# Optimization experiments

Measured on AMD Instinct MI355X. Metric: run time of the kernel, lower is better.

Reference implementation:

```python
import jax, jax.numpy as jnp
import numpy as np

N_NODES = 50000


def _mlp(h, W1, b1, W2, b2):
    return jax.nn.relu(h @ W1.T + b1) @ W2.T + b2


def _gine_layer(h, src, dst, e_emb):
    # messages: ReLU(x_src + edge_embedding), summed at destination (PyG GINEConv, eps=0)
    m = jax.nn.relu(h[src] + e_emb)                       # [E, D]
    agg = jax.ops.segment_sum(m, dst, num_segments=N_NODES)
    return h + agg                                         # (1+eps)*x + agg, eps=0


def setup_inputs() -> dict:
    key = jax.random.key(0)
    ks = jax.random.split(key, 20)
    N, E = N_NODES, 800000
    in_dim, hid, edim, n_types = 64, 128, 16, 100
    s = 0.05
    inp = {
        "x": jax.random.normal(ks[0], (N, in_dim), jnp.float32),
        "edge_index": jax.random.randint(ks[1], (2, E), 0, N, jnp.int64),
        "edge_attr": jax.random.normal(ks[2], (E, edim), jnp.float32),
        "edge_weights": jax.random.uniform(ks[3], (E,), jnp.float32),
        # layer 1: edge lin edim->in_dim, node MLP in_dim->hid->hid
        "We1": jax.random.normal(ks[4], (in_dim, edim), jnp.float32) * s,
        "be1": jnp.zeros((in_dim,), jnp.float32),
        "W11": jax.random.normal(ks[5], (hid, in_dim), jnp.float32) * s,
        "b11": jnp.zeros((hid,), jnp.float32),
        "W12": jax.random.normal(ks[6], (hid, hid), jnp.float32) * s,
        "b12": jnp.zeros((hid,), jnp.float32),
        # layer 2: edge lin edim->hid, node MLP hid->hid->hid
        "We2": jax.random.normal(ks[7], (hid, edim), jnp.float32) * s,
        "be2": jnp.zeros((hid,), jnp.float32),
        "W21": jax.random.normal(ks[8], (hid, hid), jnp.float32) * s,
        "b21": jnp.zeros((hid,), jnp.float32),
        "W22": jax.random.normal(ks[9], (hid, hid), jnp.float32) * s,
        "b22": jnp.zeros((hid,), jnp.float32),
        # output head hid -> n_atom_types
        "Wo": jax.random.normal(ks[10], (n_types, hid), jnp.float32) * s,
        "bo": jnp.zeros((n_types,), jnp.float32),
    }
    return inp


def reference(x, edge_index, edge_attr, edge_weights,
              We1, be1, W11, b11, W12, b12,
              We2, be2, W21, b21, W22, b22,
              Wo, bo):
    src, dst = edge_index[0], edge_index[1]
    ea = edge_attr * edge_weights[:, None]                 # per-edge scaling
    # layer 1
    h = _gine_layer(x, src, dst, ea @ We1.T + be1)
    h = jax.nn.relu(_mlp(h, W11, b11, W12, b12))
    # layer 2
    h = _gine_layer(h, src, dst, ea @ We2.T + be2)
    h = jax.nn.relu(_mlp(h, W21, b21, W22, b22))
    return h @ Wo.T + bo
```

## Files before the change

### kernel.cpp

```cpp
#include <hip/hip_runtime.h>

#define N_NODES 50000
#define E_EDGES 800000
#define SCAN_NB 196

__global__ __launch_bounds__(256) void k_hist(
    const int* __restrict__ ei, int* __restrict__ cnt)
{
    const int e = blockIdx.x * 256 + threadIdx.x;
    if (e < E_EDGES) atomicAdd(&cnt[ei[E_EDGES + e]], 1);
}

__global__ __launch_bounds__(256) void k_scan1(
    const int* __restrict__ cnt, int* __restrict__ bsum)
{
    __shared__ int red[256];
    const int tid = threadIdx.x;
    const int i = blockIdx.x * 256 + tid;
    red[tid] = (i < N_NODES) ? cnt[i] : 0;
    __syncthreads();
    for (int off = 128; off > 0; off >>= 1) {
        if (tid < off) red[tid] += red[tid + off];
        __syncthreads();
    }
    if (tid == 0) bsum[blockIdx.x] = red[0];
}

__global__ __launch_bounds__(256) void k_scan2(
    const int* __restrict__ bsum, int* __restrict__ boff)
{
    __shared__ int part[256];
    const int tid = threadIdx.x;
    const int v = (tid < SCAN_NB) ? bsum[tid] : 0;
    part[tid] = v;
    __syncthreads();
    for (int off = 1; off < 256; off <<= 1) {
        const int vv = part[tid];
        const int u = (tid >= off) ? part[tid - off] : 0;
        __syncthreads();
        part[tid] = vv + u;
        __syncthreads();
    }
    if (tid < SCAN_NB) boff[tid] = part[tid] - v;
}

__global__ __launch_bounds__(256) void k_scan3(
    const int* __restrict__ cnt, const int* __restrict__ boff,
    int* __restrict__ rowptr, int* __restrict__ cursor)
{
    __shared__ int part[256];
    const int tid = threadIdx.x;
    const int i = blockIdx.x * 256 + tid;
    const int v = (i < N_NODES) ? cnt[i] : 0;
    part[tid] = v;
    __syncthreads();
    for (int off = 1; off < 256; off <<= 1) {
        const int vv = part[tid];
        const int u = (tid >= off) ? part[tid - off] : 0;
        __syncthreads();
        part[tid] = vv + u;
        __syncthreads();
    }
    const int excl = part[tid] - v + boff[blockIdx.x];
    if (i < N_NODES) { rowptr[i] = excl; cursor[i] = excl; }
    if (i == N_NODES) rowptr[N_NODES] = excl;
}

__global__ __launch_bounds__(256) void k_scatter(
    const int* __restrict__ ei, int* __restrict__ cursor, int2* __restrict__ pairs)
{
    const int e = blockIdx.x * 256 + threadIdx.x;
    if (e < E_EDGES) {
        const int dst = ei[E_EDGES + e];
        const int pos = atomicAdd(&cursor[dst], 1);
        pairs[pos] = make_int2(ei[e], e);
    }
}

__global__ __launch_bounds__(256) void k_prep(
    const int2* __restrict__ pairs, const float* __restrict__ eattr,
    const float* __restrict__ ew, float* __restrict__ eaw, int* __restrict__ srcs)
{
    const int t = blockIdx.x * 256 + threadIdx.x;
    const int pos = t >> 2;
    if (pos >= E_EDGES) return;
    const int q = t & 3;
    const int2 p = pairs[pos];
    if (q == 0) srcs[pos] = p.x;
    const float w = ew[p.y];
    const float4 a = *((const float4*)(eattr + (size_t)p.y * 16) + q);
    *((float4*)(eaw + (size_t)pos * 16) + q) =
        make_float4(a.x * w, a.y * w, a.z * w, a.w * w);
}

__global__ __launch_bounds__(256) void k_wt(
    const float* __restrict__ W11, const float* __restrict__ W12,
    const float* __restrict__ W21, const float* __restrict__ W22,
    const float* __restrict__ Wo,
    const float* __restrict__ We1, const float* __restrict__ We2,
    float* __restrict__ WT)
{
    const int bid = blockIdx.x;
    const int tid = threadIdx.x;
    if (bid < 288) {
        const float* src; int KIN, JOUT, lbase, obase;
        if (bid < 32)       { src = W11; KIN = 64;  JOUT = 128; lbase = 0;   obase = 0; }
        else if (bid < 96)  { src = W12; KIN = 128; JOUT = 128; lbase = 32;  obase = 8192; }
        else if (bid < 160) { src = W21; KIN = 128; JOUT = 128; lbase = 96;  obase = 24576; }
        else if (bid < 224) { src = W22; KIN = 128; JOUT = 128; lbase = 160; obase = 40960; }
        else                { src = Wo;  KIN = 128; JOUT = 100; lbase = 224; obase = 57344; }
        const int idx = (bid - lbase) * 256 + tid;
        const int k = idx >> 7, j = idx & 127;
        WT[obase + idx] = (j < JOUT) ? src[j * KIN + k] : 0.f;
    } else if (bid < 292) {
        const int idx = (bid - 288) * 256 + tid;
        const int k = idx >> 6, d = idx & 63;
        WT[73728 + idx] = We1[d * 16 + k];
    } else {
        const int idx = (bid - 292) * 256 + tid;
        const int k = idx >> 7, d = idx & 127;
        WT[74752 + idx] = We2[d * 16 + k];
    }
}

__global__ __launch_bounds__(256, 4) void k_edge1(
    const int* __restrict__ rp, const int* __restrict__ srcs,
    const float* __restrict__ eaw,
    const float* __restrict__ WeT1, const float* __restrict__ be1,
    const float* __restrict__ x, float* __restrict__ out)
{
    const int lane = threadIdx.x & 63;
    const int node =
        __builtin_amdgcn_readfirstlane(blockIdx.x * 4 + (threadIdx.x >> 6));
    if (node >= N_NODES) return;

    float wr[16];
#pragma unroll
    for (int k = 0; k < 16; ++k) wr[k] = WeT1[k * 64 + lane];
    const float bias = be1[lane];

    const int beg = rp[node], end = rp[node + 1];
    float acc = 0.f;

#pragma unroll 4
    for (int c = beg; c < end; ++c) {
        const int src = srcs[c];
        const float hv = x[(size_t)src * 64 + lane];
        const float* ep = eaw + (size_t)c * 16;
        float d = bias;
#pragma unroll
        for (int k = 0; k < 16; ++k) d = fmaf(ep[k], wr[k], d);
        acc += fmaxf(hv + d, 0.f);
    }
    out[(size_t)node * 64 + lane] = x[(size_t)node * 64 + lane] + acc;
}

__global__ __launch_bounds__(256, 4) void k_edge2(
    const int* __restrict__ rp, const int* __restrict__ srcs,
    const float* __restrict__ eaw,
    const float* __restrict__ WeT2, const float* __restrict__ be2,
    const float* __restrict__ h, float* __restrict__ out)
{
    const int lane = threadIdx.x & 63;
    const int node =
        __builtin_amdgcn_readfirstlane(blockIdx.x * 4 + (threadIdx.x >> 6));
    if (node >= N_NODES) return;

    const int dA = 2 * lane;
    float wrA[16], wrB[16];
#pragma unroll
    for (int k = 0; k < 16; ++k) {
        const float2 w = *(const float2*)(WeT2 + k * 128 + dA);
        wrA[k] = w.x; wrB[k] = w.y;
    }
    const float2 bv = *(const float2*)(be2 + dA);
    const float biasA = bv.x, biasB = bv.y;

    const int beg = rp[node], end = rp[node + 1];
    float accA = 0.f, accB = 0.f;

    const float* hrow = h + dA;

#pragma unroll 4
    for (int c = beg; c < end; ++c) {
        const int src = srcs[c];
        const float2 hv = *(const float2*)(hrow + (size_t)src * 128);
        const float* ep = eaw + (size_t)c * 16;
        float dA_ = biasA, dB_ = biasB;
#pragma unroll
        for (int k = 0; k < 16; ++k) {
            dA_ = fmaf(ep[k], wrA[k], dA_);
            dB_ = fmaf(ep[k], wrB[k], dB_);
        }
        accA += fmaxf(hv.x + dA_, 0.f);
        accB += fmaxf(hv.y + dB_, 0.f);
    }
    const float2 self = *(const float2*)(h + (size_t)node * 128 + dA);
    *(float2*)(out + (size_t)node * 128 + dA) =
        make_float2(self.x + accA, self.y + accB);
}


#define MLP_STAGE(WTb, Bb, KIN, SRC, ACC)                                     \
    {                                                                         \
        _Pragma("unroll")                                                     \
        for (int m = 0; m < 32; ++m) ACC[m] = 0.f;                            \
        float wc[32];                                                         \
        _Pragma("unroll")                                                     \
        for (int m = 0; m < 32; ++m) wc[m] = WTb[j0 + m];                     \
        float h0 = SRC[lane];                                                 \
        for (int k = 0; k < (KIN) - 1; ++k) {                                 \
            float wn[32];                                                     \
            _Pragma("unroll")                                                 \
            for (int m = 0; m < 32; ++m) wn[m] = WTb[(k + 1) * 128 + j0 + m]; \
            const float h0n = SRC[(k + 1) * 65 + lane];                       \
            _Pragma("unroll")                                                 \
            for (int m = 0; m < 32; ++m) ACC[m] = fmaf(h0, wc[m], ACC[m]);    \
            _Pragma("unroll")                                                 \
            for (int m = 0; m < 32; ++m) wc[m] = wn[m];                       \
            h0 = h0n;                                                         \
        }                                                                     \
        _Pragma("unroll")                                                     \
        for (int m = 0; m < 32; ++m) ACC[m] = fmaf(h0, wc[m], ACC[m]);        \
    }

#define MLP_TILE(H, KIN, S)                                                   \
    for (int idx = tid; idx < 64 * ((KIN) / 4); idx += 256) {                 \
        const int q = idx & ((KIN) / 4 - 1);                                  \
        const int n = idx / ((KIN) / 4);                                      \
        const int ng = (base + n < N_NODES) ? (base + n) : (N_NODES - 1);     \
        const float4 v = *(const float4*)(H + (size_t)ng * (KIN) + 4 * q);    \
        S[(4 * q + 0) * 65 + n] = v.x;                                        \
        S[(4 * q + 1) * 65 + n] = v.y;                                        \
        S[(4 * q + 2) * 65 + n] = v.z;                                        \
        S[(4 * q + 3) * 65 + n] = v.w;                                        \
    }

__global__ __launch_bounds__(256) void k_mlp2(
    const float* __restrict__ H, const float* __restrict__ WT11,
    const float* __restrict__ b11, const float* __restrict__ WT12,
    const float* __restrict__ b12, float* __restrict__ OUT)
{
    extern __shared__ float lds[];
    float* A = lds;
    float* B = lds + 64 * 65;
    const int tid  = threadIdx.x;
    const int lane = tid & 63;
    const int j0   = __builtin_amdgcn_readfirstlane(tid >> 6) * 32;
    const int base = blockIdx.x * 64;

    MLP_TILE(H, 64, A);
    __syncthreads();

    float acc[32];
    MLP_STAGE(WT11, b11, 64, A, acc);
#pragma unroll
    for (int m = 0; m < 32; ++m)
        B[(j0 + m) * 65 + lane] = fmaxf(acc[m] + b11[j0 + m], 0.f);
    __syncthreads();

    MLP_STAGE(WT12, b12, 128, B, acc);

    const int node = base + lane;
    if (node < N_NODES) {
        float* row = OUT + (size_t)node * 128 + j0;
#pragma unroll
        for (int g = 0; g < 8; ++g) {
            float4 v;
            v.x = fmaxf(acc[4 * g + 0] + b12[j0 + 4 * g + 0], 0.f);
            v.y = fmaxf(acc[4 * g + 1] + b12[j0 + 4 * g + 1], 0.f);
            v.z = fmaxf(acc[4 * g + 2] + b12[j0 + 4 * g + 2], 0.f);
            v.w = fmaxf(acc[4 * g + 3] + b12[j0 + 4 * g + 3], 0.f);
            *(float4*)(row + 4 * g) = v;
        }
    }
}

__global__ __launch_bounds__(256) void k_mlp3(
    const float* __restrict__ H, const float* __restrict__ WT21,
    const float* __restrict__ b21, const float* __restrict__ WT22,
    const float* __restrict__ b22, const float* __restrict__ WTo,
    const float* __restrict__ bo, float* __restrict__ OUT)
{
    extern __shared__ float lds[];
    float* A = lds;
    float* B = lds + 128 * 65;
    const int tid  = threadIdx.x;
    const int lane = tid & 63;
    const int j0   = __builtin_amdgcn_readfirstlane(tid >> 6) * 32;
    const int base = blockIdx.x * 64;

    MLP_TILE(H, 128, A);
    __syncthreads();

    float acc[32];
    MLP_STAGE(WT21, b21, 128, A, acc);
#pragma unroll
    for (int m = 0; m < 32; ++m)
        B[(j0 + m) * 65 + lane] = fmaxf(acc[m] + b21[j0 + m], 0.f);
    __syncthreads();

    MLP_STAGE(WT22, b22, 128, B, acc);
    __syncthreads();
#pragma unroll
    for (int m = 0; m < 32; ++m)
        A[(j0 + m) * 65 + lane] = fmaxf(acc[m] + b22[j0 + m], 0.f);
    __syncthreads();

    MLP_STAGE(WTo, bo, 128, A, acc);

    const int node = base + lane;
    if (node < N_NODES) {
        float* row = OUT + (size_t)node * 100;
#pragma unroll
        for (int g = 0; g < 8; ++g) {
            if (j0 + 4 * g < 100) {
                float4 v;
                v.x = acc[4 * g + 0] + bo[j0 + 4 * g + 0];
                v.y = acc[4 * g + 1] + bo[j0 + 4 * g + 1];
                v.z = acc[4 * g + 2] + bo[j0 + 4 * g + 2];
                v.w = acc[4 * g + 3] + bo[j0 + 4 * g + 3];
                *(float4*)(row + j0 + 4 * g) = v;
            }
        }
    }
}

extern "C" void kernel_launch(void* const* d_in, const int* in_sizes, int n_in,
                              void* d_out, int out_size, void* d_ws, size_t ws_size,
                              hipStream_t stream) {
    const float* x     = (const float*)d_in[0];
    const int*   ei    = (const int*)  d_in[1];
    const float* eattr = (const float*)d_in[2];
    const float* ew    = (const float*)d_in[3];
    const float* We1   = (const float*)d_in[4];
    const float* be1   = (const float*)d_in[5];
    const float* W11   = (const float*)d_in[6];
    const float* b11   = (const float*)d_in[7];
    const float* W12   = (const float*)d_in[8];
    const float* b12   = (const float*)d_in[9];
    const float* We2   = (const float*)d_in[10];
    const float* be2   = (const float*)d_in[11];
    const float* W21   = (const float*)d_in[12];
    const float* b21   = (const float*)d_in[13];
    const float* W22   = (const float*)d_in[14];
    const float* b22   = (const float*)d_in[15];
    const float* Wo    = (const float*)d_in[16];
    const float* bo    = (const float*)d_in[17];
    float* out = (float*)d_out;

    char* ws = (char*)d_ws;
    int*   rowptr = (int*)  (ws + 0);
    int*   cnt    = (int*)  (ws + 204800);
    int*   cursor = (int*)  (ws + 409600);
    int*   srcs   = (int*)  (ws + 204800);
    float* eaw    = (float*)(ws + 3404800);
    float* t1     = (float*)(ws + 54604800);
    int2*  pairs  = (int2*) (ws + 54604800);
    float* h2pre  = (float*)(ws + 80204800);
    float* h1pre  = (float*)(ws + 80204800);
    float* WT     = (float*)(ws + 105804800);
    float* WT11 = WT;
    float* WT12 = WT + 8192;
    float* WT21 = WT + 24576;
    float* WT22 = WT + 40960;
    float* WTo  = WT + 57344;
    float* WeT1 = WT + 73728;
    float* WeT2 = WT + 74752;
    int*   bsum = (int*)(ws + 106116096);
    int*   boff = (int*)(ws + 106117120);

    hipMemsetAsync(cnt, 0, 200000, stream);

    k_wt<<<300, 256, 0, stream>>>(W11, W12, W21, W22, Wo, We1, We2, WT);

    const int EB = (E_EDGES + 255) / 256;
    k_hist<<<EB, 256, 0, stream>>>(ei, cnt);
    k_scan1<<<SCAN_NB, 256, 0, stream>>>(cnt, bsum);
    k_scan2<<<1, 256, 0, stream>>>(bsum, boff);
    k_scan3<<<SCAN_NB, 256, 0, stream>>>(cnt, boff, rowptr, cursor);
    k_scatter<<<EB, 256, 0, stream>>>(ei, cursor, pairs);

    const int PB = (E_EDGES * 4 + 255) / 256;
    k_prep<<<PB, 256, 0, stream>>>(pairs, eattr, ew, eaw, srcs);

    const int NB = (N_NODES + 3) / 4;
    k_edge1<<<NB, 256, 0, stream>>>(rowptr, srcs, eaw, WeT1, be1, x, h1pre);

    const int MB = (N_NODES + 63) / 64;
    const size_t ldsA = (size_t)(64 * 65 + 128 * 65) * 4;
    const size_t ldsB = (size_t)(128 * 65 + 128 * 65) * 4;

    k_mlp2<<<MB, 256, ldsA, stream>>>(h1pre, WT11, b11, WT12, b12, t1);

    k_edge2<<<NB, 256, 0, stream>>>(rowptr, srcs, eaw, WeT2, be2, t1, h2pre);

    k_mlp3<<<MB, 256, ldsB, stream>>>(h2pre, WT21, b21, WT22, b22, WTo, bo, out);
}
```

Baseline: 550.9 us.

## Process 128 nodes per MLP block, reusing weight loads across two node halves

The MLP kernels now handle 128 nodes per block instead of 64, with each thread holding two 32-wide accumulator sets so each weight value loaded from global memory feeds two FMAs. The LDS layout shrinks to a single 128x129 buffer reused in place, with extra barriers before each in-place write-back. This halves weight traffic per node and the number of blocks, at the cost of higher register pressure (64 accumulators plus the prefetch arrays), which may lower occupancy or cause spills.

Result: faster. 524.9 us (-4.7%).

```diff
diff --git a/kernel.cpp b/kernel.cpp
--- a/kernel.cpp
+++ b/kernel.cpp
@@ -201,39 +201,54 @@
 }
 
 
-#define MLP_STAGE(WTb, Bb, KIN, SRC, ACC)                                     \
+#define MLP_STAGE2(WTb, KIN, S, A0, A1)                                       \
     {                                                                         \
         _Pragma("unroll")                                                     \
-        for (int m = 0; m < 32; ++m) ACC[m] = 0.f;                            \
+        for (int m = 0; m < 32; ++m) { A0[m] = 0.f; A1[m] = 0.f; }            \
         float wc[32];                                                         \
         _Pragma("unroll")                                                     \
         for (int m = 0; m < 32; ++m) wc[m] = WTb[j0 + m];                     \
-        float h0 = SRC[lane];                                                 \
+        float h0 = S[lane], h1 = S[lane + 64];                                \
         for (int k = 0; k < (KIN) - 1; ++k) {                                 \
             float wn[32];                                                     \
             _Pragma("unroll")                                                 \
             for (int m = 0; m < 32; ++m) wn[m] = WTb[(k + 1) * 128 + j0 + m]; \
-            const float h0n = SRC[(k + 1) * 65 + lane];                       \
+            const float h0n = S[(k + 1) * 129 + lane];                        \
+            const float h1n = S[(k + 1) * 129 + lane + 64];                   \
             _Pragma("unroll")                                                 \
-            for (int m = 0; m < 32; ++m) ACC[m] = fmaf(h0, wc[m], ACC[m]);    \
+            for (int m = 0; m < 32; ++m) {                                    \
+                A0[m] = fmaf(h0, wc[m], A0[m]);                               \
+                A1[m] = fmaf(h1, wc[m], A1[m]);                               \
+            }                                                                 \
             _Pragma("unroll")                                                 \
             for (int m = 0; m < 32; ++m) wc[m] = wn[m];                       \
-            h0 = h0n;                                                         \
+            h0 = h0n; h1 = h1n;                                               \
         }                                                                     \
         _Pragma("unroll")                                                     \
-        for (int m = 0; m < 32; ++m) ACC[m] = fmaf(h0, wc[m], ACC[m]);        \
-    }
-
-#define MLP_TILE(H, KIN, S)                                                   \
-    for (int idx = tid; idx < 64 * ((KIN) / 4); idx += 256) {                 \
+        for (int m = 0; m < 32; ++m) {                                        \
+            A0[m] = fmaf(h0, wc[m], A0[m]);                                   \
+            A1[m] = fmaf(h1, wc[m], A1[m]);                                   \
+        }                                                                     \
+    }
+
+#define MLP_TILE128(H, KIN, S)                                                \
+    for (int idx = tid; idx < 128 * ((KIN) / 4); idx += 256) {                \
         const int q = idx & ((KIN) / 4 - 1);                                  \
         const int n = idx / ((KIN) / 4);                                      \
         const int ng = (base + n < N_NODES) ? (base + n) : (N_NODES - 1);     \
         const float4 v = *(const float4*)(H + (size_t)ng * (KIN) + 4 * q);    \
-        S[(4 * q + 0) * 65 + n] = v.x;                                        \
-        S[(4 * q + 1) * 65 + n] = v.y;                                        \
-        S[(4 * q + 2) * 65 + n] = v.z;                                        \
-        S[(4 * q + 3) * 65 + n] = v.w;                                        \
+        S[(4 * q + 0) * 129 + n] = v.x;                                       \
+        S[(4 * q + 1) * 129 + n] = v.y;                                       \
+        S[(4 * q + 2) * 129 + n] = v.z;                                       \
+        S[(4 * q + 3) * 129 + n] = v.w;                                       \
+    }
+
+#define MLP_WRITE_LDS(S, Bb, A0, A1)                                          \
+    _Pragma("unroll")                                                         \
+    for (int m = 0; m < 32; ++m) {                                            \
+        const float bb = Bb[j0 + m];                                          \
+        S[(j0 + m) * 129 + lane]      = fmaxf(A0[m] + bb, 0.f);               \
+        S[(j0 + m) * 129 + lane + 64] = fmaxf(A1[m] + bb, 0.f);               \
     }
 
 __global__ __launch_bounds__(256) void k_mlp2(
@@ -241,36 +256,45 @@
     const float* __restrict__ b11, const float* __restrict__ WT12,
     const float* __restrict__ b12, float* __restrict__ OUT)
 {
-    extern __shared__ float lds[];
-    float* A = lds;
-    float* B = lds + 64 * 65;
+    extern __shared__ float S[];
     const int tid  = threadIdx.x;
     const int lane = tid & 63;
     const int j0   = __builtin_amdgcn_readfirstlane(tid >> 6) * 32;
-    const int base = blockIdx.x * 64;
-
-    MLP_TILE(H, 64, A);
-    __syncthreads();
-
-    float acc[32];
-    MLP_STAGE(WT11, b11, 64, A, acc);
-#pragma unroll
-    for (int m = 0; m < 32; ++m)
-        B[(j0 + m) * 65 + lane] = fmaxf(acc[m] + b11[j0 + m], 0.f);
-    __syncthreads();
-
-    MLP_STAGE(WT12, b12, 128, B, acc);
-
-    const int node = base + lane;
-    if (node < N_NODES) {
-        float* row = OUT + (size_t)node * 128 + j0;
+    const int base = blockIdx.x * 128;
+
+    MLP_TILE128(H, 64, S);
+    __syncthreads();
+
+    float acc0[32], acc1[32];
+    MLP_STAGE2(WT11, 64, S, acc0, acc1);
+    __syncthreads();
+    MLP_WRITE_LDS(S, b11, acc0, acc1);
+    __syncthreads();
+
+    MLP_STAGE2(WT12, 128, S, acc0, acc1);
+
+    const int n0 = base + lane, n1 = base + lane + 64;
+    if (n0 < N_NODES) {
+        float* row = OUT + (size_t)n0 * 128 + j0;
 #pragma unroll
         for (int g = 0; g < 8; ++g) {
             float4 v;
-            v.x = fmaxf(acc[4 * g + 0] + b12[j0 + 4 * g + 0], 0.f);
-            v.y = fmaxf(acc[4 * g + 1] + b12[j0 + 4 * g + 1], 0.f);
-            v.z = fmaxf(acc[4 * g + 2] + b12[j0 + 4 * g + 2], 0.f);
-            v.w = fmaxf(acc[4 * g + 3] + b12[j0 + 4 * g + 3], 0.f);
+            v.x = fmaxf(acc0[4 * g + 0] + b12[j0 + 4 * g + 0], 0.f);
+            v.y = fmaxf(acc0[4 * g + 1] + b12[j0 + 4 * g + 1], 0.f);
+            v.z = fmaxf(acc0[4 * g + 2] + b12[j0 + 4 * g + 2], 0.f);
+            v.w = fmaxf(acc0[4 * g + 3] + b12[j0 + 4 * g + 3], 0.f);
+            *(float4*)(row + 4 * g) = v;
+        }
+    }
+    if (n1 < N_NODES) {
+        float* row = OUT + (size_t)n1 * 128 + j0;
+#pragma unroll
+        for (int g = 0; g < 8; ++g) {
+            float4 v;
+            v.x = fmaxf(acc1[4 * g + 0] + b12[j0 + 4 * g + 0], 0.f);
+            v.y = fmaxf(acc1[4 * g + 1] + b12[j0 + 4 * g + 1], 0.f);
+            v.z = fmaxf(acc1[4 * g + 2] + b12[j0 + 4 * g + 2], 0.f);
+            v.w = fmaxf(acc1[4 * g + 3] + b12[j0 + 4 * g + 3], 0.f);
             *(float4*)(row + 4 * g) = v;
         }
     }
@@ -282,44 +306,53 @@
     const float* __restrict__ b22, const float* __restrict__ WTo,
     const float* __restrict__ bo, float* __restrict__ OUT)
 {
-    extern __shared__ float lds[];
-    float* A = lds;
-    float* B = lds + 128 * 65;
+    extern __shared__ float S[];
     const int tid  = threadIdx.x;
     const int lane = tid & 63;
     const int j0   = __builtin_amdgcn_readfirstlane(tid >> 6) * 32;
-    const int base = blockIdx.x * 64;
-
-    MLP_TILE(H, 128, A);
-    __syncthreads();
-
-    float acc[32];
-    MLP_STAGE(WT21, b21, 128, A, acc);
-#pragma unroll
-    for (int m = 0; m < 32; ++m)
-        B[(j0 + m) * 65 + lane] = fmaxf(acc[m] + b21[j0 + m], 0.f);
-    __syncthreads();
-
-    MLP_STAGE(WT22, b22, 128, B, acc);
-    __syncthreads();
-#pragma unroll
-    for (int m = 0; m < 32; ++m)
-        A[(j0 + m) * 65 + lane] = fmaxf(acc[m] + b22[j0 + m], 0.f);
-    __syncthreads();
-
-    MLP_STAGE(WTo, bo, 128, A, acc);
-
-    const int node = base + lane;
-    if (node < N_NODES) {
-        float* row = OUT + (size_t)node * 100;
+    const int base = blockIdx.x * 128;
+
+    MLP_TILE128(H, 128, S);
+    __syncthreads();
+
+    float acc0[32], acc1[32];
+    MLP_STAGE2(WT21, 128, S, acc0, acc1);
+    __syncthreads();
+    MLP_WRITE_LDS(S, b21, acc0, acc1);
+    __syncthreads();
+
+    MLP_STAGE2(WT22, 128, S, acc0, acc1);
+    __syncthreads();
+    MLP_WRITE_LDS(S, b22, acc0, acc1);
+    __syncthreads();
+
+    MLP_STAGE2(WTo, 128, S, acc0, acc1);
+
+    const int n0 = base + lane, n1 = base + lane + 64;
+    if (n0 < N_NODES) {
+        float* row = OUT + (size_t)n0 * 100;
 #pragma unroll
         for (int g = 0; g < 8; ++g) {
             if (j0 + 4 * g < 100) {
                 float4 v;
-                v.x = acc[4 * g + 0] + bo[j0 + 4 * g + 0];
-                v.y = acc[4 * g + 1] + bo[j0 + 4 * g + 1];
-                v.z = acc[4 * g + 2] + bo[j0 + 4 * g + 2];
-                v.w = acc[4 * g + 3] + bo[j0 + 4 * g + 3];
+                v.x = acc0[4 * g + 0] + bo[j0 + 4 * g + 0];
+                v.y = acc0[4 * g + 1] + bo[j0 + 4 * g + 1];
+                v.z = acc0[4 * g + 2] + bo[j0 + 4 * g + 2];
+                v.w = acc0[4 * g + 3] + bo[j0 + 4 * g + 3];
+                *(float4*)(row + j0 + 4 * g) = v;
+            }
+        }
+    }
+    if (n1 < N_NODES) {
+        float* row = OUT + (size_t)n1 * 100;
+#pragma unroll
+        for (int g = 0; g < 8; ++g) {
+            if (j0 + 4 * g < 100) {
+                float4 v;
+                v.x = acc1[4 * g + 0] + bo[j0 + 4 * g + 0];
+                v.y = acc1[4 * g + 1] + bo[j0 + 4 * g + 1];
+                v.z = acc1[4 * g + 2] + bo[j0 + 4 * g + 2];
+                v.w = acc1[4 * g + 3] + bo[j0 + 4 * g + 3];
                 *(float4*)(row + j0 + 4 * g) = v;
             }
         }
@@ -387,13 +420,12 @@
     const int NB = (N_NODES + 3) / 4;
     k_edge1<<<NB, 256, 0, stream>>>(rowptr, srcs, eaw, WeT1, be1, x, h1pre);
 
-    const int MB = (N_NODES + 63) / 64;
-    const size_t ldsA = (size_t)(64 * 65 + 128 * 65) * 4;
-    const size_t ldsB = (size_t)(128 * 65 + 128 * 65) * 4;
-
-    k_mlp2<<<MB, 256, ldsA, stream>>>(h1pre, WT11, b11, WT12, b12, t1);
+    const int MB = (N_NODES + 127) / 128;
+    const size_t ldsS = (size_t)(128 * 129) * 4;
+
+    k_mlp2<<<MB, 256, ldsS, stream>>>(h1pre, WT11, b11, WT12, b12, t1);
 
     k_edge2<<<NB, 256, 0, stream>>>(rowptr, srcs, eaw, WeT2, be2, t1, h2pre);
 
-    k_mlp3<<<MB, 256, ldsB, stream>>>(h2pre, WT21, b21, WT22, b22, WTo, bo, out);
-}
+    k_mlp3<<<MB, 256, ldsS, stream>>>(h2pre, WT21, b21, WT22, b22, WTo, bo, out);
+}
```

## Enlarge MLP node tiles to 128 per block and reuse one LDS buffer in place

Applied to the files above, without the earlier changes.

The MLP kernels now process 128 nodes per block with 512 threads (8 waves: 4 output-column groups by 2 node halves) instead of 64 nodes with 256 threads. The two separate LDS buffers are merged into one 128x129 array that is overwritten in place, with an extra barrier before each write so every wave has finished reading. This amortizes the per-block weight loads over twice as many nodes and cuts LDS use per node, which should allow better occupancy. The cost is more barriers and larger blocks, which could hurt scheduling or raise register pressure under the 512,4 launch bound.

Measured after the change: 501.8 us. -8.9%, faster.

```diff
diff --git a/kernel.cpp b/kernel.cpp
--- a/kernel.cpp
+++ b/kernel.cpp
@@ -201,19 +201,19 @@
 }
 
 
-#define MLP_STAGE(WTb, Bb, KIN, SRC, ACC)                                     \
+#define MLP_STAGE1(WTb, KIN, S, ACC)                                          \
     {                                                                         \
         _Pragma("unroll")                                                     \
         for (int m = 0; m < 32; ++m) ACC[m] = 0.f;                            \
         float wc[32];                                                         \
         _Pragma("unroll")                                                     \
         for (int m = 0; m < 32; ++m) wc[m] = WTb[j0 + m];                     \
-        float h0 = SRC[lane];                                                 \
+        float h0 = S[nb + lane];                                              \
         for (int k = 0; k < (KIN) - 1; ++k) {                                 \
             float wn[32];                                                     \
             _Pragma("unroll")                                                 \
             for (int m = 0; m < 32; ++m) wn[m] = WTb[(k + 1) * 128 + j0 + m]; \
-            const float h0n = SRC[(k + 1) * 65 + lane];                       \
+            const float h0n = S[(k + 1) * 129 + nb + lane];                   \
             _Pragma("unroll")                                                 \
             for (int m = 0; m < 32; ++m) ACC[m] = fmaf(h0, wc[m], ACC[m]);    \
             _Pragma("unroll")                                                 \
@@ -224,44 +224,48 @@
         for (int m = 0; m < 32; ++m) ACC[m] = fmaf(h0, wc[m], ACC[m]);        \
     }
 
-#define MLP_TILE(H, KIN, S)                                                   \
-    for (int idx = tid; idx < 64 * ((KIN) / 4); idx += 256) {                 \
+#define MLP_TILE128(H, KIN, S)                                                \
+    for (int idx = tid; idx < 128 * ((KIN) / 4); idx += 512) {                \
         const int q = idx & ((KIN) / 4 - 1);                                  \
         const int n = idx / ((KIN) / 4);                                      \
         const int ng = (base + n < N_NODES) ? (base + n) : (N_NODES - 1);     \
         const float4 v = *(const float4*)(H + (size_t)ng * (KIN) + 4 * q);    \
-        S[(4 * q + 0) * 65 + n] = v.x;                                        \
-        S[(4 * q + 1) * 65 + n] = v.y;                                        \
-        S[(4 * q + 2) * 65 + n] = v.z;                                        \
-        S[(4 * q + 3) * 65 + n] = v.w;                                        \
-    }
-
-__global__ __launch_bounds__(256) void k_mlp2(
+        S[(4 * q + 0) * 129 + n] = v.x;                                       \
+        S[(4 * q + 1) * 129 + n] = v.y;                                       \
+        S[(4 * q + 2) * 129 + n] = v.z;                                       \
+        S[(4 * q + 3) * 129 + n] = v.w;                                       \
+    }
+
+#define MLP_WRITE_LDS(S, Bb, ACC)                                             \
+    _Pragma("unroll")                                                         \
+    for (int m = 0; m < 32; ++m)                                              \
+        S[(j0 + m) * 129 + nb + lane] = fmaxf(ACC[m] + Bb[j0 + m], 0.f);
+
+__global__ __launch_bounds__(512, 4) void k_mlp2(
     const float* __restrict__ H, const float* __restrict__ WT11,
     const float* __restrict__ b11, const float* __restrict__ WT12,
     const float* __restrict__ b12, float* __restrict__ OUT)
 {
-    extern __shared__ float lds[];
-    float* A = lds;
-    float* B = lds + 64 * 65;
+    extern __shared__ float S[];
     const int tid  = threadIdx.x;
     const int lane = tid & 63;
-    const int j0   = __builtin_amdgcn_readfirstlane(tid >> 6) * 32;
-    const int base = blockIdx.x * 64;
-
-    MLP_TILE(H, 64, A);
+    const int wv   = __builtin_amdgcn_readfirstlane(tid >> 6);
+    const int j0   = (wv & 3) * 32;
+    const int nb   = (wv >> 2) * 64;
+    const int base = blockIdx.x * 128;
+
+    MLP_TILE128(H, 64, S);
     __syncthreads();
 
     float acc[32];
-    MLP_STAGE(WT11, b11, 64, A, acc);
-#pragma unroll
-    for (int m = 0; m < 32; ++m)
-        B[(j0 + m) * 65 + lane] = fmaxf(acc[m] + b11[j0 + m], 0.f);
-    __syncthreads();
-
-    MLP_STAGE(WT12, b12, 128, B, acc);
-
-    const int node = base + lane;
+    MLP_STAGE1(WT11, 64, S, acc);
+    __syncthreads();
+    MLP_WRITE_LDS(S, b11, acc);
+    __syncthreads();
+
+    MLP_STAGE1(WT12, 128, S, acc);
+
+    const int node = base + nb + lane;
     if (node < N_NODES) {
         float* row = OUT + (size_t)node * 128 + j0;
 #pragma unroll
@@ -276,40 +280,37 @@
     }
 }
 
-__global__ __launch_bounds__(256) void k_mlp3(
+__global__ __launch_bounds__(512, 4) void k_mlp3(
     const float* __restrict__ H, const float* __restrict__ WT21,
     const float* __restrict__ b21, const float* __restrict__ WT22,
     const float* __restrict__ b22, const float* __restrict__ WTo,
     const float* __restrict__ bo, float* __restrict__ OUT)
 {
-    extern __shared__ float lds[];
-    float* A = lds;
-    float* B = lds + 128 * 65;
+    extern __shared__ float S[];
     const int tid  = threadIdx.x;
     const int lane = tid & 63;
-    const int j0   = __builtin_amdgcn_readfirstlane(tid >> 6) * 32;
-    const int base = blockIdx.x * 64;
-
-    MLP_TILE(H, 128, A);
+    const int wv   = __builtin_amdgcn_readfirstlane(tid >> 6);
+    const int j0   = (wv & 3) * 32;
+    const int nb   = (wv >> 2) * 64;
+    const int base = blockIdx.x * 128;
+
+    MLP_TILE128(H, 128, S);
     __syncthreads();
 
     float acc[32];
-    MLP_STAGE(WT21, b21, 128, A, acc);
-#pragma unroll
-    for (int m = 0; m < 32; ++m)
-        B[(j0 + m) * 65 + lane] = fmaxf(acc[m] + b21[j0 + m], 0.f);
-    __syncthreads();
-
-    MLP_STAGE(WT22, b22, 128, B, acc);
-    __syncthreads();
-#pragma unroll
-    for (int m = 0; m < 32; ++m)
-        A[(j0 + m) * 65 + lane] = fmaxf(acc[m] + b22[j0 + m], 0.f);
-    __syncthreads();
-
-    MLP_STAGE(WTo, bo, 128, A, acc);
-
-    const int node = base + lane;
+    MLP_STAGE1(WT21, 128, S, acc);
+    __syncthreads();
+    MLP_WRITE_LDS(S, b21, acc);
+    __syncthreads();
+
+    MLP_STAGE1(WT22, 128, S, acc);
+    __syncthreads();
+    MLP_WRITE_LDS(S, b22, acc);
+    __syncthreads();
+
+    MLP_STAGE1(WTo, 128, S, acc);
+
+    const int node = base + nb + lane;
     if (node < N_NODES) {
         float* row = OUT + (size_t)node * 100;
 #pragma unroll
@@ -387,13 +388,12 @@
     const int NB = (N_NODES + 3) / 4;
     k_edge1<<<NB, 256, 0, stream>>>(rowptr, srcs, eaw, WeT1, be1, x, h1pre);
 
-    const int MB = (N_NODES + 63) / 64;
-    const size_t ldsA = (size_t)(64 * 65 + 128 * 65) * 4;
-    const size_t ldsB = (size_t)(128 * 65 + 128 * 65) * 4;
-
-    k_mlp2<<<MB, 256, ldsA, stream>>>(h1pre, WT11, b11, WT12, b12, t1);
+    const int MB = (N_NODES + 127) / 128;
+    const size_t ldsS = (size_t)(128 * 129) * 4;
+
+    k_mlp2<<<MB, 512, ldsS, stream>>>(h1pre, WT11, b11, WT12, b12, t1);
 
     k_edge2<<<NB, 256, 0, stream>>>(rowptr, srcs, eaw, WeT2, be2, t1, h2pre);
 
-    k_mlp3<<<MB, 256, ldsB, stream>>>(h2pre, WT21, b21, WT22, b22, WTo, bo, out);
-}
+    k_mlp3<<<MB, 512, ldsS, stream>>>(h2pre, WT21, b21, WT22, b22, WTo, bo, out);
+}
```
